# Kernel tuning notes

Measured on AMD Instinct MI355X. Metric: run time of the kernel, lower is better.

The kernel has to match this reference:

```python
import jax, jax.numpy as jnp
import numpy as np

N_NODES = 100000
N_EDGES = 1600000
IN_C, HID_C, OUT_C = 128, 128, 64
EPS = 1e-12


def _glorot(key, shape):
    fan_in, fan_out = shape
    lim = (6.0 / (fan_in + fan_out)) ** 0.5
    return jax.random.uniform(key, shape, jnp.float32, -lim, lim)


def setup_inputs() -> dict:
    key = jax.random.key(0)
    ks = jax.random.split(key, 12)
    x = jax.random.normal(ks[0], (N_NODES, IN_C), jnp.float32)
    edge_index = jax.random.randint(ks[1], (2, N_EDGES), 0, N_NODES, jnp.int64)
    dims = [(IN_C, HID_C), (HID_C, HID_C), (HID_C, OUT_C)]
    inp = {"x": x, "edge_index": edge_index}
    for i, (din, dout) in enumerate(dims):
        inp[f"Wl{i}"] = _glorot(ks[2 + 3 * i], (din, dout))          # lin_l weight (neighbor path, has bias)
        inp[f"bl{i}"] = jnp.zeros((dout,), jnp.float32)               # lin_l bias
        inp[f"Wr{i}"] = _glorot(ks[3 + 3 * i], (din, dout))          # lin_r weight (root path, no bias)
    return inp


def sage_conv(x, src, dst, Wl, bl, Wr):
    # mean aggregation of neighbor features onto destination nodes
    msgs = x[src]                                                     # [E, d] gather
    agg = jax.ops.segment_sum(msgs, dst, num_segments=N_NODES)       # [N, d] scatter-add
    deg = jax.ops.segment_sum(jnp.ones((src.shape[0],), x.dtype), dst, num_segments=N_NODES)
    mean = agg / jnp.maximum(deg, 1.0)[:, None]
    out = mean @ Wl + bl + x @ Wr
    # normalize=True -> L2 normalize per node
    nrm = jnp.linalg.norm(out, axis=-1, keepdims=True)
    return out / jnp.maximum(nrm, EPS)


def reference(x, edge_index, Wl0, bl0, Wr0, Wl1, bl1, Wr1, Wl2, bl2, Wr2):
    src, dst = edge_index[0], edge_index[1]
    h = sage_conv(x, src, dst, Wl0, bl0, Wr0)
    h = jax.nn.relu(h)  # dropout is identity in eval mode
    h = sage_conv(h, src, dst, Wl1, bl1, Wr1)
    h = jax.nn.relu(h)
    h = sage_conv(h, src, dst, Wl2, bl2, Wr2)
    return h
```

## Files before the change

kernel.cpp:

```cpp
#include <hip/hip_runtime.h>
#include <math.h>


typedef __attribute__((ext_vector_type(8))) short short8;
typedef __attribute__((ext_vector_type(4))) float f32x4;
typedef __attribute__((ext_vector_type(2))) float f32x2;

#define BSHIFT 9
#define BSIZE 512
#define MAXBUCK 224
#define P1_EDGES 8192
#define P1_CAP 64
#define CAPB 10240
#define GPAD 16

#define XSCALE 64.0f
#define HSCALE 256.0f

__device__ __forceinline__ unsigned f2bf_rtn(float f) {
    unsigned u = __float_as_uint(f);
    return (u + 0x7fffu + ((u >> 16) & 1u)) >> 16;
}
__device__ __forceinline__ float bf_lo(unsigned v) { return __uint_as_float(v << 16); }
__device__ __forceinline__ float bf_hi(unsigned v) { return __uint_as_float(v & 0xffff0000u); }


__global__ __launch_bounds__(256) void partition_edges(const int* __restrict__ src,
                                                       const int* __restrict__ dst, int E,
                                                       int NBUCK,
                                                       unsigned* __restrict__ recs,
                                                       int* __restrict__ gcntp) {
    __shared__ int cnt[MAXBUCK];
    __shared__ int basem[MAXBUCK];
    __shared__ unsigned rec[MAXBUCK * P1_CAP];
    const int tid = threadIdx.x;
    for (int i = tid; i < NBUCK; i += 256) cnt[i] = 0;
    __syncthreads();

    const int base = blockIdx.x * P1_EDGES;
#pragma unroll
    for (int r = 0; r < P1_EDGES / 1024; r++) {
        int e = base + r * 1024 + tid * 4;
        if (e + 3 < E) {
            int4 s4 = *(const int4*)(src + e);
            int4 d4 = *(const int4*)(dst + e);
            int ss[4] = {s4.x, s4.y, s4.z, s4.w};
            int dd[4] = {d4.x, d4.y, d4.z, d4.w};
#pragma unroll
            for (int j = 0; j < 4; j++) {
                int b = dd[j] >> BSHIFT;
                unsigned rr = ((unsigned)ss[j] << BSHIFT) | (unsigned)(dd[j] & (BSIZE - 1));
                int pos = atomicAdd(&cnt[b], 1);
                if (pos < P1_CAP) {
                    rec[(b << 6) + pos] = rr;
                } else {
                    int gp = atomicAdd(&gcntp[b * GPAD], 1);
                    if (gp < CAPB) recs[(size_t)b * CAPB + gp] = rr;
                }
            }
        } else {
            for (int j = 0; j < 4; j++) {
                int ee = e + j;
                if (ee < E) {
                    int s = src[ee], d = dst[ee];
                    int b = d >> BSHIFT;
                    unsigned rr = ((unsigned)s << BSHIFT) | (unsigned)(d & (BSIZE - 1));
                    int pos = atomicAdd(&cnt[b], 1);
                    if (pos < P1_CAP) {
                        rec[(b << 6) + pos] = rr;
                    } else {
                        int gp = atomicAdd(&gcntp[b * GPAD], 1);
                        if (gp < CAPB) recs[(size_t)b * CAPB + gp] = rr;
                    }
                }
            }
        }
    }
    __syncthreads();

    for (int b = tid; b < NBUCK; b += 256) {
        int c = min(cnt[b], P1_CAP);
        cnt[b] = c;
        basem[b] = (c > 0) ? atomicAdd(&gcntp[b * GPAD], c) : 0;
    }
    __syncthreads();

    const int quads = NBUCK << 4;
    for (int sq = tid; sq < quads; sq += 256) {
        int b = sq >> 4, i0 = (sq & 15) << 2;
        int c = cnt[b];
        if (i0 < c) {
            int gp = basem[b] + i0;
            if (i0 + 3 < c && gp + 3 < CAPB) {
                uint4 v = *(const uint4*)&rec[(b << 6) + i0];
                *(uint4*)&recs[(size_t)b * CAPB + gp] = v;
            } else {
                for (int j = 0; j < 4 && i0 + j < c; j++) {
                    if (gp + j < CAPB) recs[(size_t)b * CAPB + gp + j] = rec[(b << 6) + i0 + j];
                }
            }
        }
    }
}


__device__ __forceinline__ void pack_frag128(const float* Wl, const float* Wr,
                                             unsigned short* Bp, int idx) {
    int lane = idx & 63;
    int nt = (idx >> 6) % 8;
    int ks = (idx >> 6) / 8;
    int n = nt * 16 + (lane & 15);
    int k0 = ks * 32 + (lane >> 4) * 8;
#pragma unroll
    for (int j = 0; j < 8; j++) {
        int k = k0 + j;
        float w = (k < 128) ? Wl[k * 128 + n] : Wr[(k - 128) * 128 + n];
        Bp[(size_t)idx * 8 + j] = (unsigned short)f2bf_rtn(w);
    }
}

__device__ __forceinline__ void pack_frag2(const float* Wl, const float* Wr,
                                           unsigned short* Bp, int idx) {
    int lane = idx & 63;
    int nt = (idx >> 6) % 8;
    int ks = (idx >> 6) / 8;
    int n = nt * 16 + (lane & 15);
    int k0 = ks * 32 + (lane >> 4) * 8;
#pragma unroll
    for (int j = 0; j < 8; j++) {
        int k = k0 + j;
        float w = (n < 64) ? Wl[k * 64 + n] : Wr[k * 64 + (n - 64)];
        Bp[(size_t)idx * 8 + j] = (unsigned short)f2bf_rtn(w);
    }
}


__global__ __launch_bounds__(512) void csr_prep(const unsigned* __restrict__ recs,
                                                const int* __restrict__ gcntp,
                                                int2* __restrict__ rsdeg,
                                                int* __restrict__ srcs,
                                                const float* __restrict__ x,
                                                unsigned short* __restrict__ xbf,
                                                unsigned char* __restrict__ xq,
                                                const float* __restrict__ Wl0,
                                                const float* __restrict__ Wr0,
                                                const float* __restrict__ Wl1,
                                                const float* __restrict__ Wr1,
                                                const float* __restrict__ Wl2,
                                                const float* __restrict__ Wr2,
                                                const float* __restrict__ bl2,
                                                unsigned short* __restrict__ Bp0,
                                                unsigned short* __restrict__ Bp1,
                                                unsigned short* __restrict__ Bp2,
                                                float* __restrict__ bias2,
                                                unsigned char* __restrict__ hAq, int N,
                                                int NB, int PB) {
    const int tid = threadIdx.x;
    if (blockIdx.x < NB) {
        __shared__ int hist[512];
        __shared__ int cur[512];
        __shared__ int wtot[8];

        const int b = blockIdx.x;
        const unsigned* r = recs + (size_t)b * CAPB;
        const int cnt = min(gcntp[b * GPAD], CAPB);
        int* sb = srcs + (size_t)b * CAPB;
        const int lane = tid & 63;
        const int wave = tid >> 6;

        hist[tid] = 0;
        __syncthreads();
        for (int i = tid; i < cnt; i += 512) atomicAdd(&hist[r[i] & (BSIZE - 1)], 1);
        __syncthreads();

        const int h0 = hist[tid];
        const int v = (h0 + 3) & ~3;
        int s = v;
#pragma unroll
        for (int off = 1; off < 64; off <<= 1) {
            int t = __shfl_up(s, off, 64);
            if (lane >= off) s += t;
        }
        if (lane == 63) wtot[wave] = s;
        __syncthreads();
        if (tid < 8) {
            int wv = wtot[tid];
            int ss = wv;
#pragma unroll
            for (int off = 1; off < 8; off <<= 1) {
                int t = __shfl_up(ss, off, 8);
                if (tid >= off) ss += t;
            }
            wtot[tid] = ss - wv;
        }
        __syncthreads();
        const int ex = s - v + wtot[wave];
        cur[tid] = ex;
        __syncthreads();

        for (int i = tid; i < cnt; i += 512) {
            unsigned rr = r[i];
            int d = rr & (BSIZE - 1);
            int pos = atomicAdd(&cur[d], 1);
            if (pos < CAPB) sb[pos] = (int)(rr >> BSHIFT);
        }

        {
            int p = (h0 + 3) & ~3;
            for (int k = h0; k < p; k++)
                if (ex + k < CAPB) sb[ex + k] = N;
            const int node = (b << BSHIFT) + tid;
            if (node < N) {
                int2 rd;
                rd.x = b * CAPB + ex;
                rd.y = h0;
                rsdeg[node] = rd;
            }
        }
        return;
    }

    const int pbi = blockIdx.x - NB;
    if (pbi < PB) {
        const int l = tid & 63;
        const int w = tid >> 6;
        const int row0 = pbi * 32 + w;

        float2 v[4];
#pragma unroll
        for (int k = 0; k < 4; k++) {
            int row = row0 + 8 * k;
            float2 t = {0.f, 0.f};
            if (row < N) t = ((const float2*)x)[(size_t)row * 64 + l];
            v[k] = t;
        }

#pragma unroll
        for (int k = 0; k < 4; k++) {
            int row = row0 + 8 * k;
            if (row > N) continue;
            ((unsigned*)xbf)[(size_t)row * 64 + l] =
                f2bf_rtn(v[k].x) | (f2bf_rtn(v[k].y) << 16);
            float vv[8];
#pragma unroll
            for (int nt = 0; nt < 8; nt++) {
                int sl = 8 * nt + (l >> 1);
                float a = __shfl(v[k].x, sl, 64);
                float bb = __shfl(v[k].y, sl, 64);
                float val = ((l & 1) ? bb : a) * XSCALE;
                vv[nt] = fminf(fmaxf(val, -440.0f), 440.0f);
            }
            if (l < 16) {
                unsigned w0 = 0, w1 = 0;
                w0 = __builtin_amdgcn_cvt_pk_fp8_f32(vv[0], vv[1], w0, false);
                w0 = __builtin_amdgcn_cvt_pk_fp8_f32(vv[2], vv[3], w0, true);
                w1 = __builtin_amdgcn_cvt_pk_fp8_f32(vv[4], vv[5], w1, false);
                w1 = __builtin_amdgcn_cvt_pk_fp8_f32(vv[6], vv[7], w1, true);
                uint2 wq;
                wq.x = w0;
                wq.y = w1;
                ((uint2*)xq)[(size_t)row * 16 + l] = wq;
            }
        }
        return;
    }
    const int pb = pbi - PB;
    if (pb < 8) {
        pack_frag128(Wl0, Wr0, Bp0, pb * 512 + tid);
    } else if (pb < 16) {
        pack_frag128(Wl1, Wr1, Bp1, (pb - 8) * 512 + tid);
    } else if (pb < 20) {
        pack_frag2(Wl2, Wr2, Bp2, (pb - 16) * 512 + tid);
    } else {
        if (tid < 64) {
            bias2[tid] = 0.0f;
            bias2[64 + tid] = bl2[tid];
        } else if (tid < 96) {
            ((unsigned*)(hAq + (size_t)N * 128))[tid - 64] = 0;
        }
    }
}


__global__ __launch_bounds__(1024) void aggregate_fp8(const unsigned char* __restrict__ hq,
                                                      const int2* __restrict__ rsdeg,
                                                      const int* __restrict__ srcs,
                                                      unsigned short* __restrict__ mean,
                                                      int N, float unscale) {
    const int node = blockIdx.x * 64 + (threadIdx.x >> 4);
    if (node >= N) return;
    const int lane = threadIdx.x & 63;
    const int c = lane & 15;
    const int gb4 = (lane & 48) << 2;
    int2 rd = rsdeg[node];
    const int start = rd.x, cnt = rd.y;
    const int pcnt = (cnt + 3) & ~3;
    const uint2* hp = (const uint2*)hq;

    int sv0 = srcs[start + c];
    int sv1 = (pcnt > 16) ? srcs[start + 16 + c] : 0;
    int sv2 = (pcnt > 32) ? srcs[start + 32 + c] : 0;
    int sv3 = (pcnt > 48) ? srcs[start + 48 + c] : 0;

    f32x2 a0 = {0.f, 0.f}, a1 = {0.f, 0.f}, a2 = {0.f, 0.f}, a3 = {0.f, 0.f};

    const int pmain = (pcnt < 64) ? pcnt : 64;
    for (int e = 0; e < pmain; e += 8) {
        int sv = (e < 32) ? ((e < 16) ? sv0 : sv1) : ((e < 48) ? sv2 : sv3);
        int bidx = gb4 | ((e & 15) << 2);
        int s0 = __builtin_amdgcn_ds_bpermute(bidx, sv);
        int s1 = __builtin_amdgcn_ds_bpermute(bidx + 4, sv);
        int s2 = __builtin_amdgcn_ds_bpermute(bidx + 8, sv);
        int s3 = __builtin_amdgcn_ds_bpermute(bidx + 12, sv);
        int s4 = __builtin_amdgcn_ds_bpermute(bidx + 16, sv);
        int s5 = __builtin_amdgcn_ds_bpermute(bidx + 20, sv);
        int s6 = __builtin_amdgcn_ds_bpermute(bidx + 24, sv);
        int s7 = __builtin_amdgcn_ds_bpermute(bidx + 28, sv);
        const bool hiv = (e + 4) < pcnt;
        s4 = hiv ? s4 : N;
        s5 = hiv ? s5 : N;
        s6 = hiv ? s6 : N;
        s7 = hiv ? s7 : N;
        uint2 v0 = hp[(unsigned)(s0 << 4) + c];
        uint2 v1 = hp[(unsigned)(s1 << 4) + c];
        uint2 v2 = hp[(unsigned)(s2 << 4) + c];
        uint2 v3 = hp[(unsigned)(s3 << 4) + c];
        uint2 v4 = hp[(unsigned)(s4 << 4) + c];
        uint2 v5 = hp[(unsigned)(s5 << 4) + c];
        uint2 v6 = hp[(unsigned)(s6 << 4) + c];
        uint2 v7 = hp[(unsigned)(s7 << 4) + c];
        a0 += __builtin_amdgcn_cvt_pk_f32_fp8(v0.x, false);
        a1 += __builtin_amdgcn_cvt_pk_f32_fp8(v0.x, true);
        a2 += __builtin_amdgcn_cvt_pk_f32_fp8(v0.y, false);
        a3 += __builtin_amdgcn_cvt_pk_f32_fp8(v0.y, true);
        a0 += __builtin_amdgcn_cvt_pk_f32_fp8(v1.x, false);
        a1 += __builtin_amdgcn_cvt_pk_f32_fp8(v1.x, true);
        a2 += __builtin_amdgcn_cvt_pk_f32_fp8(v1.y, false);
        a3 += __builtin_amdgcn_cvt_pk_f32_fp8(v1.y, true);
        a0 += __builtin_amdgcn_cvt_pk_f32_fp8(v2.x, false);
        a1 += __builtin_amdgcn_cvt_pk_f32_fp8(v2.x, true);
        a2 += __builtin_amdgcn_cvt_pk_f32_fp8(v2.y, false);
        a3 += __builtin_amdgcn_cvt_pk_f32_fp8(v2.y, true);
        a0 += __builtin_amdgcn_cvt_pk_f32_fp8(v3.x, false);
        a1 += __builtin_amdgcn_cvt_pk_f32_fp8(v3.x, true);
        a2 += __builtin_amdgcn_cvt_pk_f32_fp8(v3.y, false);
        a3 += __builtin_amdgcn_cvt_pk_f32_fp8(v3.y, true);
        a0 += __builtin_amdgcn_cvt_pk_f32_fp8(v4.x, false);
        a1 += __builtin_amdgcn_cvt_pk_f32_fp8(v4.x, true);
        a2 += __builtin_amdgcn_cvt_pk_f32_fp8(v4.y, false);
        a3 += __builtin_amdgcn_cvt_pk_f32_fp8(v4.y, true);
        a0 += __builtin_amdgcn_cvt_pk_f32_fp8(v5.x, false);
        a1 += __builtin_amdgcn_cvt_pk_f32_fp8(v5.x, true);
        a2 += __builtin_amdgcn_cvt_pk_f32_fp8(v5.y, false);
        a3 += __builtin_amdgcn_cvt_pk_f32_fp8(v5.y, true);
        a0 += __builtin_amdgcn_cvt_pk_f32_fp8(v6.x, false);
        a1 += __builtin_amdgcn_cvt_pk_f32_fp8(v6.x, true);
        a2 += __builtin_amdgcn_cvt_pk_f32_fp8(v6.y, false);
        a3 += __builtin_amdgcn_cvt_pk_f32_fp8(v6.y, true);
        a0 += __builtin_amdgcn_cvt_pk_f32_fp8(v7.x, false);
        a1 += __builtin_amdgcn_cvt_pk_f32_fp8(v7.x, true);
        a2 += __builtin_amdgcn_cvt_pk_f32_fp8(v7.y, false);
        a3 += __builtin_amdgcn_cvt_pk_f32_fp8(v7.y, true);
    }
    for (int e = 64; e < pcnt; e += 4) {
        int s0 = srcs[start + e];
        int s1 = srcs[start + e + 1];
        int s2 = srcs[start + e + 2];
        int s3 = srcs[start + e + 3];
        uint2 v0 = hp[(unsigned)(s0 << 4) + c];
        uint2 v1 = hp[(unsigned)(s1 << 4) + c];
        uint2 v2 = hp[(unsigned)(s2 << 4) + c];
        uint2 v3 = hp[(unsigned)(s3 << 4) + c];
        a0 += __builtin_amdgcn_cvt_pk_f32_fp8(v0.x, false);
        a1 += __builtin_amdgcn_cvt_pk_f32_fp8(v0.x, true);
        a2 += __builtin_amdgcn_cvt_pk_f32_fp8(v0.y, false);
        a3 += __builtin_amdgcn_cvt_pk_f32_fp8(v0.y, true);
        a0 += __builtin_amdgcn_cvt_pk_f32_fp8(v1.x, false);
        a1 += __builtin_amdgcn_cvt_pk_f32_fp8(v1.x, true);
        a2 += __builtin_amdgcn_cvt_pk_f32_fp8(v1.y, false);
        a3 += __builtin_amdgcn_cvt_pk_f32_fp8(v1.y, true);
        a0 += __builtin_amdgcn_cvt_pk_f32_fp8(v2.x, false);
        a1 += __builtin_amdgcn_cvt_pk_f32_fp8(v2.x, true);
        a2 += __builtin_amdgcn_cvt_pk_f32_fp8(v2.y, false);
        a3 += __builtin_amdgcn_cvt_pk_f32_fp8(v2.y, true);
        a0 += __builtin_amdgcn_cvt_pk_f32_fp8(v3.x, false);
        a1 += __builtin_amdgcn_cvt_pk_f32_fp8(v3.x, true);
        a2 += __builtin_amdgcn_cvt_pk_f32_fp8(v3.y, false);
        a3 += __builtin_amdgcn_cvt_pk_f32_fp8(v3.y, true);
    }

    f32x2 b0, b1, b2, b3;
    b0.x = __shfl_xor(a0.x, 1, 64); b0.y = __shfl_xor(a0.y, 1, 64);
    b1.x = __shfl_xor(a1.x, 1, 64); b1.y = __shfl_xor(a1.y, 1, 64);
    b2.x = __shfl_xor(a2.x, 1, 64); b2.y = __shfl_xor(a2.y, 1, 64);
    b3.x = __shfl_xor(a3.x, 1, 64); b3.y = __shfl_xor(a3.y, 1, 64);
    if ((c & 1) == 0) {
        const float inv = unscale / fmaxf((float)cnt, 1.0f);
        unsigned* mw = (unsigned*)mean + (size_t)node * 64 + (c >> 1);
        mw[0]  = f2bf_rtn(a0.x * inv) | (f2bf_rtn(b0.x * inv) << 16);
        mw[8]  = f2bf_rtn(a0.y * inv) | (f2bf_rtn(b0.y * inv) << 16);
        mw[16] = f2bf_rtn(a1.x * inv) | (f2bf_rtn(b1.x * inv) << 16);
        mw[24] = f2bf_rtn(a1.y * inv) | (f2bf_rtn(b1.y * inv) << 16);
        mw[32] = f2bf_rtn(a2.x * inv) | (f2bf_rtn(b2.x * inv) << 16);
        mw[40] = f2bf_rtn(a2.y * inv) | (f2bf_rtn(b2.y * inv) << 16);
        mw[48] = f2bf_rtn(a3.x * inv) | (f2bf_rtn(b3.x * inv) << 16);
        mw[56] = f2bf_rtn(a3.y * inv) | (f2bf_rtn(b3.y * inv) << 16);
    }
}


__global__ __launch_bounds__(1024) void agg64_norm(const unsigned short* __restrict__ z2,
                                                   const int2* __restrict__ rsdeg,
                                                   const int* __restrict__ srcs,
                                                   float* __restrict__ out, int N) {
    const int node = blockIdx.x * 128 + (threadIdx.x >> 3);
    if (node >= N) return;
    const int lane = threadIdx.x & 63;
    const int c = lane & 7;
    const int gb4 = (lane & 56) << 2;
    int2 rd = rsdeg[node];
    const int start = rd.x, cnt = rd.y;
    const int pcnt = (cnt + 3) & ~3;
    const uint4* hp = (const uint4*)z2;

    int sv0 = srcs[start + c];
    int sv1 = (pcnt > 8) ? srcs[start + 8 + c] : 0;
    int sv2 = (pcnt > 16) ? srcs[start + 16 + c] : 0;
    int sv3 = (pcnt > 24) ? srcs[start + 24 + c] : 0;

    float a[8] = {0.f, 0.f, 0.f, 0.f, 0.f, 0.f, 0.f, 0.f};

    const int pmain = (pcnt < 32) ? pcnt : 32;
    for (int e = 0; e < pmain; e += 2) {
        int sv = (e < 16) ? ((e < 8) ? sv0 : sv1) : ((e < 24) ? sv2 : sv3);
        int bidx = gb4 | ((e & 7) << 2);
        int s0 = __builtin_amdgcn_ds_bpermute(bidx, sv);
        int s1 = __builtin_amdgcn_ds_bpermute(bidx + 4, sv);
        uint4 v0 = hp[(unsigned)(s0 << 4) + c];
        uint4 v1 = hp[(unsigned)(s1 << 4) + c];
        a[0] += bf_lo(v0.x); a[1] += bf_hi(v0.x);
        a[2] += bf_lo(v0.y); a[3] += bf_hi(v0.y);
        a[4] += bf_lo(v0.z); a[5] += bf_hi(v0.z);
        a[6] += bf_lo(v0.w); a[7] += bf_hi(v0.w);
        a[0] += bf_lo(v1.x); a[1] += bf_hi(v1.x);
        a[2] += bf_lo(v1.y); a[3] += bf_hi(v1.y);
        a[4] += bf_lo(v1.z); a[5] += bf_hi(v1.z);
        a[6] += bf_lo(v1.w); a[7] += bf_hi(v1.w);
    }
    for (int e = 32; e < pcnt; e += 2) {
        int s0 = srcs[start + e];
        int s1 = srcs[start + e + 1];
        uint4 v0 = hp[(unsigned)(s0 << 4) + c];
        uint4 v1 = hp[(unsigned)(s1 << 4) + c];
        a[0] += bf_lo(v0.x); a[1] += bf_hi(v0.x);
        a[2] += bf_lo(v0.y); a[3] += bf_hi(v0.y);
        a[4] += bf_lo(v0.z); a[5] += bf_hi(v0.z);
        a[6] += bf_lo(v0.w); a[7] += bf_hi(v0.w);
        a[0] += bf_lo(v1.x); a[1] += bf_hi(v1.x);
        a[2] += bf_lo(v1.y); a[3] += bf_hi(v1.y);
        a[4] += bf_lo(v1.z); a[5] += bf_hi(v1.z);
        a[6] += bf_lo(v1.w); a[7] += bf_hi(v1.w);
    }

    const float inv = 1.0f / fmaxf((float)cnt, 1.0f);
    uint4 r = hp[(unsigned)(node << 4) + 8 + c];
    float vv[8];
    vv[0] = a[0] * inv + bf_lo(r.x); vv[1] = a[1] * inv + bf_hi(r.x);
    vv[2] = a[2] * inv + bf_lo(r.y); vv[3] = a[3] * inv + bf_hi(r.y);
    vv[4] = a[4] * inv + bf_lo(r.z); vv[5] = a[5] * inv + bf_hi(r.z);
    vv[6] = a[6] * inv + bf_lo(r.w); vv[7] = a[7] * inv + bf_hi(r.w);
    float ss = 0.f;
#pragma unroll
    for (int i = 0; i < 8; i++) ss += vv[i] * vv[i];
    ss += __shfl_xor(ss, 1, 64);
    ss += __shfl_xor(ss, 2, 64);
    ss += __shfl_xor(ss, 4, 64);
    const float rinv = 1.0f / fmaxf(sqrtf(ss), 1e-12f);
    float4 o0 = {vv[0] * rinv, vv[1] * rinv, vv[2] * rinv, vv[3] * rinv};
    float4 o1 = {vv[4] * rinv, vv[5] * rinv, vv[6] * rinv, vv[7] * rinv};
    ((float4*)out)[(size_t)node * 16 + 2 * c] = o0;
    ((float4*)out)[(size_t)node * 16 + 2 * c + 1] = o1;
}


template <int KT, int DOUT, int RELU, int NORM, int BF16OUT, int EMITFP8>
__global__ __launch_bounds__(512) void sage_gemm(const unsigned short* __restrict__ meanb,
                                                 const unsigned short* __restrict__ hb,
                                                 const unsigned short* __restrict__ Bp,
                                                 const float* __restrict__ bias,
                                                 void* __restrict__ outp,
                                                 unsigned char* __restrict__ hq, int N) {
    constexpr int NT = DOUT / 16;
    constexpr int MT = 2;
    __shared__ short Bl[KT * NT * 64 * 8];

    const int tid = threadIdx.x;
    {
        const uint4* s = (const uint4*)Bp;
        uint4* d = (uint4*)Bl;
        constexpr int CNT = KT * NT * 64;
        for (int i = tid; i < CNT; i += 512) d[i] = s[i];
    }
    __syncthreads();

    const int wave = tid >> 6;
    const int lane = tid & 63;
    const int m = lane & 15;
    const int q = lane >> 4;
    const int rowbase = blockIdx.x * (128 * MT);

    int rowA[MT];
#pragma unroll
    for (int t = 0; t < MT; t++) rowA[t] = rowbase + (wave * MT + t) * 16 + m;

    f32x4 acc[MT][NT];
#pragma unroll
    for (int t = 0; t < MT; t++)
#pragma unroll
        for (int nt = 0; nt < NT; nt++) acc[t][nt] = (f32x4)0.0f;

#pragma unroll
    for (int ks = 0; ks < KT; ks++) {
        const unsigned short* ab = (KT == 8) ? ((ks < 4) ? meanb : hb) : hb;
        const int koff = (KT == 8 ? (ks & 3) : ks) * 32 + q * 8;
        short8 afrag[MT];
#pragma unroll
        for (int t = 0; t < MT; t++) {
            if (rowA[t] < N)
                afrag[t] = *(const short8*)(ab + (size_t)rowA[t] * 128 + koff);
            else
                afrag[t] = (short8)(short)0;
        }
#pragma unroll
        for (int nt = 0; nt < NT; nt++) {
            short8 bfrag = *(const short8*)&Bl[((ks * NT + nt) * 64 + lane) * 8];
#pragma unroll
            for (int t = 0; t < MT; t++)
                acc[t][nt] = __builtin_amdgcn_mfma_f32_16x16x32_bf16(afrag[t], bfrag,
                                                                     acc[t][nt], 0, 0, 0);
        }
    }

    float bs[NT];
#pragma unroll
    for (int nt = 0; nt < NT; nt++) bs[nt] = bias[nt * 16 + m];

#pragma unroll
    for (int t = 0; t < MT; t++) {
        float rinv[4] = {1.f, 1.f, 1.f, 1.f};
#pragma unroll
        for (int nt = 0; nt < NT; nt++)
#pragma unroll
            for (int r = 0; r < 4; r++) acc[t][nt][r] += bs[nt];
        if (NORM) {
            float ss[4] = {0.f, 0.f, 0.f, 0.f};
#pragma unroll
            for (int nt = 0; nt < NT; nt++)
#pragma unroll
                for (int r = 0; r < 4; r++) ss[r] += acc[t][nt][r] * acc[t][nt][r];
#pragma unroll
            for (int msk = 1; msk < 16; msk <<= 1)
#pragma unroll
                for (int r = 0; r < 4; r++) ss[r] += __shfl_xor(ss[r], msk, 64);
#pragma unroll
            for (int r = 0; r < 4; r++) rinv[r] = 1.0f / fmaxf(sqrtf(ss[r]), 1e-12f);
        }

#pragma unroll
        for (int r = 0; r < 4; r++) {
            int row = rowbase + (wave * MT + t) * 16 + q * 4 + r;
            if (row < N) {
                float vv[NT];
#pragma unroll
                for (int nt = 0; nt < NT; nt++) {
                    float v = acc[t][nt][r];
                    if (NORM) v *= rinv[r];
                    if (RELU) v = fmaxf(v, 0.0f);
                    vv[nt] = v;
                    int col = nt * 16 + m;
                    if (BF16OUT)
                        ((unsigned short*)outp)[(size_t)row * DOUT + col] =
                            (unsigned short)f2bf_rtn(v);
                    else
                        ((float*)outp)[(size_t)row * DOUT + col] = v;
                }
                if constexpr (EMITFP8) {
                    unsigned w0 = 0, w1 = 0;
                    w0 = __builtin_amdgcn_cvt_pk_fp8_f32(vv[0] * HSCALE, vv[1] * HSCALE, w0, false);
                    w0 = __builtin_amdgcn_cvt_pk_fp8_f32(vv[2] * HSCALE, vv[3] * HSCALE, w0, true);
                    w1 = __builtin_amdgcn_cvt_pk_fp8_f32(vv[4] * HSCALE, vv[5] * HSCALE, w1, false);
                    w1 = __builtin_amdgcn_cvt_pk_fp8_f32(vv[6] * HSCALE, vv[7] * HSCALE, w1, true);
                    uint2 wq;
                    wq.x = w0;
                    wq.y = w1;
                    ((uint2*)hq)[(size_t)row * 16 + m] = wq;
                }
            }
        }
    }
}

static inline size_t align_up(size_t x, size_t a) { return (x + a - 1) & ~(a - 1); }

extern "C" void kernel_launch(void* const* d_in, const int* in_sizes, int n_in,
                              void* d_out, int out_size, void* d_ws, size_t ws_size,
                              hipStream_t stream) {
    const int N = in_sizes[0] / 128;
    const int E = in_sizes[1] / 2;
    const int NBUCK = (N + BSIZE - 1) >> BSHIFT;

    const float* x = (const float*)d_in[0];
    const int* ei = (const int*)d_in[1];
    const int* src = ei;
    const int* dst = ei + E;
    const float* Wl0 = (const float*)d_in[2];
    const float* bl0 = (const float*)d_in[3];
    const float* Wr0 = (const float*)d_in[4];
    const float* Wl1 = (const float*)d_in[5];
    const float* bl1 = (const float*)d_in[6];
    const float* Wr1 = (const float*)d_in[7];
    const float* Wl2 = (const float*)d_in[8];
    const float* bl2 = (const float*)d_in[9];
    const float* Wr2 = (const float*)d_in[10];
    float* out = (float*)d_out;

    char* w = (char*)d_ws;
    int2* rsdeg = (int2*)w;             w += align_up((size_t)N * 8, 256);
    int* gcntp = (int*)w;               w += align_up((size_t)MAXBUCK * GPAD * 4, 256);
    unsigned* recs = (unsigned*)w;      w += align_up((size_t)NBUCK * CAPB * 4, 256);
    int* srcs = (int*)w;                w += align_up((size_t)NBUCK * CAPB * 4, 256);
    unsigned short* xbf = (unsigned short*)w;  w += align_up((size_t)(N + 1) * 128 * 2, 256);
    unsigned char* xq = (unsigned char*)w;     w += align_up((size_t)(N + 1) * 128, 256);
    unsigned char* hAq = (unsigned char*)w;    w += align_up((size_t)(N + 1) * 128, 256);
    unsigned short* hA = (unsigned short*)w;   w += align_up((size_t)N * 128 * 2, 256);
    unsigned short* hB = (unsigned short*)w;   w += align_up((size_t)N * 128 * 2, 256);
    unsigned short* meanb = (unsigned short*)w; w += align_up((size_t)N * 128 * 2, 256);
    unsigned short* Bp0 = (unsigned short*)w;  w += align_up(8 * 8 * 64 * 8 * 2, 256);
    unsigned short* Bp1 = (unsigned short*)w;  w += align_up(8 * 8 * 64 * 8 * 2, 256);
    unsigned short* Bp2 = (unsigned short*)w;  w += align_up(4 * 8 * 64 * 8 * 2, 256);
    float* bias2 = (float*)w;                  w += align_up(128 * 4, 256);
    unsigned short* z2 = xbf;

    const int PB = (N + 32) / 32;
    const int NB = NBUCK;

    hipMemsetAsync(gcntp, 0, (size_t)MAXBUCK * GPAD * 4, stream);
    partition_edges<<<(E + P1_EDGES - 1) / P1_EDGES, 256, 0, stream>>>(src, dst, E, NBUCK,
                                                                       recs, gcntp);
    csr_prep<<<NB + PB + 21, 512, 0, stream>>>(recs, gcntp, rsdeg, srcs, x, xbf, xq,
                                               Wl0, Wr0, Wl1, Wr1, Wl2, Wr2, bl2,
                                               Bp0, Bp1, Bp2, bias2, hAq, N, NB, PB);

    const int aggGrid = (N + 63) / 64;
    const int aggGrid128 = (N + 127) / 128;
    const int gemmGrid = (N + 255) / 256;

    aggregate_fp8<<<aggGrid, 1024, 0, stream>>>(xq, rsdeg, srcs, meanb, N, 1.0f / XSCALE);
    sage_gemm<8, 128, 1, 1, 1, 1><<<gemmGrid, 512, 0, stream>>>(meanb, xbf, Bp0, bl0, hA,
                                                                hAq, N);

    aggregate_fp8<<<aggGrid, 1024, 0, stream>>>(hAq, rsdeg, srcs, meanb, N, 1.0f / HSCALE);
    sage_gemm<8, 128, 1, 1, 1, 0><<<gemmGrid, 512, 0, stream>>>(meanb, hA, Bp1, bl1, hB,
                                                                nullptr, N);

    sage_gemm<4, 128, 0, 0, 1, 0><<<gemmGrid, 512, 0, stream>>>(hB, hB, Bp2, bias2, z2,
                                                                nullptr, N);
    agg64_norm<<<aggGrid128, 1024, 0, stream>>>(z2, rsdeg, srcs, out, N);
}
```

Measured before the change: 306.3 us.

## Fuse layer-1 GEMM/normalize/ReLU with layer-2 projection GEMM in one kernel

Adds a kernel that computes the layer-1 GEMM with bias, L2 normalization and ReLU, then keeps the 256-row hidden tile in shared memory (XOR-swizzled bf16) and feeds it straight into the layer-2 projection GEMM. This removes the write and read of the hB intermediate in global memory and one kernel launch. In exchange it reuses the weight LDS buffer for the hidden tile, adds extra barriers, and reads the layer-2 weights directly from global memory rather than from LDS.

```diff
diff --git a/kernel.cpp b/kernel.cpp
--- a/kernel.cpp
+++ b/kernel.cpp
@@ -600,6 +600,146 @@
     }
 }
 
+
+__global__ __launch_bounds__(512) void sage_gemm12(const unsigned short* __restrict__ meanb,
+                                                   const unsigned short* __restrict__ hA,
+                                                   const unsigned short* __restrict__ Bp1,
+                                                   const float* __restrict__ bl1,
+                                                   const unsigned short* __restrict__ Bp2,
+                                                   const float* __restrict__ bias2,
+                                                   unsigned short* __restrict__ z2, int N) {
+    __shared__ short Bl[8 * 8 * 64 * 8];
+
+    const int tid = threadIdx.x;
+    {
+        const uint4* s = (const uint4*)Bp1;
+        uint4* d = (uint4*)Bl;
+        for (int i = tid; i < 8 * 8 * 64; i += 512) d[i] = s[i];
+    }
+    __syncthreads();
+
+    const int wave = tid >> 6;
+    const int lane = tid & 63;
+    const int m = lane & 15;
+    const int q = lane >> 4;
+    const int rowbase = blockIdx.x * 256;
+
+    int rowA[2];
+#pragma unroll
+    for (int t = 0; t < 2; t++) rowA[t] = rowbase + (wave * 2 + t) * 16 + m;
+
+    f32x4 acc[2][8];
+#pragma unroll
+    for (int t = 0; t < 2; t++)
+#pragma unroll
+        for (int nt = 0; nt < 8; nt++) acc[t][nt] = (f32x4)0.0f;
+
+#pragma unroll
+    for (int ks = 0; ks < 8; ks++) {
+        const unsigned short* ab = (ks < 4) ? meanb : hA;
+        const int koff = (ks & 3) * 32 + q * 8;
+        short8 afrag[2];
+#pragma unroll
+        for (int t = 0; t < 2; t++) {
+            if (rowA[t] < N)
+                afrag[t] = *(const short8*)(ab + (size_t)rowA[t] * 128 + koff);
+            else
+                afrag[t] = (short8)(short)0;
+        }
+#pragma unroll
+        for (int nt = 0; nt < 8; nt++) {
+            short8 bfrag = *(const short8*)&Bl[((ks * 8 + nt) * 64 + lane) * 8];
+#pragma unroll
+            for (int t = 0; t < 2; t++)
+                acc[t][nt] = __builtin_amdgcn_mfma_f32_16x16x32_bf16(afrag[t], bfrag,
+                                                                     acc[t][nt], 0, 0, 0);
+        }
+    }
+
+    float bs1[8];
+#pragma unroll
+    for (int nt = 0; nt < 8; nt++) bs1[nt] = bl1[nt * 16 + m];
+
+    __syncthreads();
+
+#pragma unroll
+    for (int t = 0; t < 2; t++) {
+#pragma unroll
+        for (int nt = 0; nt < 8; nt++)
+#pragma unroll
+            for (int r = 0; r < 4; r++) acc[t][nt][r] += bs1[nt];
+        float ssr[4] = {0.f, 0.f, 0.f, 0.f};
+#pragma unroll
+        for (int nt = 0; nt < 8; nt++)
+#pragma unroll
+            for (int r = 0; r < 4; r++) ssr[r] += acc[t][nt][r] * acc[t][nt][r];
+#pragma unroll
+        for (int msk = 1; msk < 16; msk <<= 1)
+#pragma unroll
+            for (int r = 0; r < 4; r++) ssr[r] += __shfl_xor(ssr[r], msk, 64);
+        float rinv[4];
+#pragma unroll
+        for (int r = 0; r < 4; r++) rinv[r] = 1.0f / fmaxf(sqrtf(ssr[r]), 1e-12f);
+
+#pragma unroll
+        for (int r = 0; r < 4; r++) {
+            const int lr = (wave * 2 + t) * 16 + q * 4 + r;
+#pragma unroll
+            for (int nt = 0; nt < 8; nt++) {
+                float v = fmaxf(acc[t][nt][r] * rinv[r], 0.0f);
+                const int col = nt * 16 + m;
+                const int boff = (lr * 256 + col * 2) ^ ((lr & 7) << 4);
+                *(unsigned short*)((char*)Bl + boff) = (unsigned short)f2bf_rtn(v);
+            }
+        }
+    }
+    __syncthreads();
+
+    f32x4 acc2[2][8];
+#pragma unroll
+    for (int t = 0; t < 2; t++)
+#pragma unroll
+        for (int nt = 0; nt < 8; nt++) acc2[t][nt] = (f32x4)0.0f;
+
+#pragma unroll
+    for (int ks = 0; ks < 4; ks++) {
+        short8 af2[2];
+#pragma unroll
+        for (int t = 0; t < 2; t++) {
+            const int lr = (wave * 2 + t) * 16 + m;
+            const int boff = (lr * 256 + ks * 64 + q * 16) ^ ((lr & 7) << 4);
+            af2[t] = *(const short8*)((const char*)Bl + boff);
+        }
+#pragma unroll
+        for (int nt = 0; nt < 8; nt++) {
+            short8 bf2 = *(const short8*)(Bp2 + (size_t)((ks * 8 + nt) * 64 + lane) * 8);
+#pragma unroll
+            for (int t = 0; t < 2; t++)
+                acc2[t][nt] = __builtin_amdgcn_mfma_f32_16x16x32_bf16(af2[t], bf2,
+                                                                      acc2[t][nt], 0, 0, 0);
+        }
+    }
+
+    float bs2[8];
+#pragma unroll
+    for (int nt = 0; nt < 8; nt++) bs2[nt] = bias2[nt * 16 + m];
+
+#pragma unroll
+    for (int t = 0; t < 2; t++) {
+#pragma unroll
+        for (int r = 0; r < 4; r++) {
+            int row = rowbase + (wave * 2 + t) * 16 + q * 4 + r;
+            if (row < N) {
+#pragma unroll
+                for (int nt = 0; nt < 8; nt++) {
+                    float v = acc2[t][nt][r] + bs2[nt];
+                    z2[(size_t)row * 128 + nt * 16 + m] = (unsigned short)f2bf_rtn(v);
+                }
+            }
+        }
+    }
+}
+
 static inline size_t align_up(size_t x, size_t a) { return (x + a - 1) & ~(a - 1); }
 
 extern "C" void kernel_launch(void* const* d_in, const int* in_sizes, int n_in,
@@ -640,6 +780,7 @@
     unsigned short* Bp2 = (unsigned short*)w;  w += align_up(4 * 8 * 64 * 8 * 2, 256);
     float* bias2 = (float*)w;                  w += align_up(128 * 4, 256);
     unsigned short* z2 = xbf;
+    (void)hB;
 
     const int PB = (N + 32) / 32;
     const int NB = NBUCK;
@@ -660,10 +801,7 @@
                                                                 hAq, N);
 
     aggregate_fp8<<<aggGrid, 1024, 0, stream>>>(hAq, rsdeg, srcs, meanb, N, 1.0f / HSCALE);
-    sage_gemm<8, 128, 1, 1, 1, 0><<<gemmGrid, 512, 0, stream>>>(meanb, hA, Bp1, bl1, hB,
-                                                                nullptr, N);
-
-    sage_gemm<4, 128, 0, 0, 1, 0><<<gemmGrid, 512, 0, stream>>>(hB, hB, Bp2, bias2, z2,
-                                                                nullptr, N);
+    sage_gemm12<<<gemmGrid, 512, 0, stream>>>(meanb, hA, Bp1, bl1, Bp2, bias2, z2, N);
+
     agg64_norm<<<aggGrid128, 1024, 0, stream>>>(z2, rsdeg, srcs, out, N);
 }
```

New measurement: 294.0 us. -4.0%, faster.
